# Optimization experiments

Measured on AMD Instinct MI355X. Metric: run time of the kernel, lower is better.

## Reference

```python
import jax, jax.numpy as jnp
import numpy as np

RANK = 8
LN_EPS = 1e-5


def setup_inputs() -> dict:
    key = jax.random.key(0)
    ks = jax.random.split(key, 8)
    B, T, D = 16, 1024, 1024
    A = 1024          # ada_dim
    I = 1024          # inter_dim
    OUT = D * RANK * 4  # 32768
    s = 0.02
    return {
        "x": jax.random.normal(ks[0], (B, T, D), jnp.float32),
        "ada_emb": jax.random.normal(ks[1], (B, A), jnp.float32),
        "base_up": jax.random.normal(ks[2], (D, D), jnp.float32) * s,
        "base_down": jax.random.normal(ks[3], (D, D), jnp.float32) * s,
        "ln_gamma": jnp.ones((A,), jnp.float32),
        "ln_beta": jnp.zeros((A,), jnp.float32),
        "W1": jax.random.normal(ks[4], (A, I), jnp.float32) / np.sqrt(A),
        "bias1": jnp.zeros((I,), jnp.float32),
        "W2": jax.random.normal(ks[5], (I, OUT), jnp.float32) / np.sqrt(I),
        "bias2": jnp.zeros((OUT,), jnp.float32),
    }


def reference(x, ada_emb, base_up, base_down, ln_gamma, ln_beta, W1, bias1, W2, bias2):
    B, T, D = x.shape
    R = RANK
    # norm_cond: LayerNorm over ada_dim (biased variance, eps=1e-5)
    mu = jnp.mean(ada_emb, axis=-1, keepdims=True)
    var = jnp.mean(jnp.square(ada_emb - mu), axis=-1, keepdims=True)
    c = (ada_emb - mu) / jnp.sqrt(var + LN_EPS) * ln_gamma + ln_beta
    # gen_weight: Linear -> GELU -> Linear
    h = jax.nn.gelu(c @ W1 + bias1, approximate=False)
    w = h @ W2 + bias2                         # (B, 4*D*R)
    a1, b1, a2, b2 = [t.reshape(B, D, R) for t in jnp.split(w, 4, axis=-1)]
    # down matvec: x @ (base_down + a2 @ b2^T), factored to avoid (B,D,D)
    u = jnp.einsum('btd,bdr->btr', x, a2)      # (B,T,R)
    mid = jnp.einsum('btd,dl->btl', x, base_down) + jnp.einsum('btr,blr->btl', u, b2)
    mid = jax.nn.gelu(mid, approximate=False)  # act_fn between layers
    # up matvec: (base_up + a1 @ b1^T) @ mid, factored
    v = jnp.einsum('blr,btl->btr', b1, mid)    # (B,T,R)
    out = jnp.einsum('btl,kl->btk', mid, base_up) + jnp.einsum('bkr,btr->btk', a1, v)
    return x + out  # residual
```

## Files before the change

### kernel.cpp

```cpp
#include <hip/hip_runtime.h>
#include <math.h>

#define DD 1024
#define NB 16
#define WSPLIT 8
#define HSPLIT 32

typedef unsigned short u16;
typedef __attribute__((ext_vector_type(8))) short short8;
typedef __attribute__((ext_vector_type(4))) float f32x4;

__device__ __forceinline__ float gelu_f(float x) {
  return 0.5f * x * (1.0f + erff(x * 0.70710678118654752440f));
}
__device__ __forceinline__ u16 f2bf(float f) {
  union { float f; unsigned u; } v; v.f = f;
  return (u16)((v.u + 0x7FFFu + ((v.u >> 16) & 1u)) >> 16);
}
__device__ __forceinline__ float bf2f(u16 b) {
  union { unsigned u; float f; } v; v.u = ((unsigned)b) << 16;
  return v.f;
}
__device__ __forceinline__ void gload_lds16(const u16* g, u16* l) {
  __builtin_amdgcn_global_load_lds(
      (const __attribute__((address_space(1))) void*)g,
      (__attribute__((address_space(3))) void*)l, 16, 0, 0);
}
__device__ __forceinline__ void gload_lds16f(const float* g, float* l) {
  __builtin_amdgcn_global_load_lds(
      (const __attribute__((address_space(1))) void*)g,
      (__attribute__((address_space(3))) void*)l, 16, 0, 0);
}

#define VMCNT8   asm volatile("s_waitcnt vmcnt(8)" ::: "memory")
#define VMCNT4   asm volatile("s_waitcnt vmcnt(4)" ::: "memory")
#define VMCNT0   asm volatile("s_waitcnt vmcnt(0)" ::: "memory")
#define BARRIER  asm volatile("s_barrier" ::: "memory")

__launch_bounds__(256)
__global__ void prep_kernel(const float* __restrict__ x, u16* __restrict__ xb,
                            const float* __restrict__ ada, const float* __restrict__ gamma,
                            const float* __restrict__ beta, float* __restrict__ c,
                            const float* __restrict__ bdn, u16* __restrict__ bdTb,
                            const float* __restrict__ bu, u16* __restrict__ bub) {
  __shared__ float smem[1056];
  int bid = blockIdx.x;
  int t = threadIdx.x;
  if (bid < 8192) {
    size_t i = (size_t)bid * 256 + t;
    const float4* xf = (const float4*)x;
    float4 v0 = xf[i * 2], v1 = xf[i * 2 + 1];
    short8 o;
    o[0] = (short)f2bf(v0.x); o[1] = (short)f2bf(v0.y);
    o[2] = (short)f2bf(v0.z); o[3] = (short)f2bf(v0.w);
    o[4] = (short)f2bf(v1.x); o[5] = (short)f2bf(v1.y);
    o[6] = (short)f2bf(v1.z); o[7] = (short)f2bf(v1.w);
    *(short8*)(xb + i * 8) = o;
  } else if (bid < 8208) {
    int b = bid - 8192;
    const float* row = ada + b * DD;
    float s = 0.f, s2 = 0.f;
    for (int i = t; i < DD; i += 256) { float v = row[i]; s += v; s2 += v * v; }
    for (int off = 32; off; off >>= 1) { s += __shfl_down(s, off); s2 += __shfl_down(s2, off); }
    float* rs = smem; float* rs2 = smem + 4;
    int wave = t >> 6, lane = t & 63;
    if (lane == 0) { rs[wave] = s; rs2[wave] = s2; }
    __syncthreads();
    if (t == 0) {
      float a = 0.f, a2 = 0.f;
      for (int w = 0; w < 4; w++) { a += rs[w]; a2 += rs2[w]; }
      rs[0] = a * (1.0f / DD); rs2[0] = a2 * (1.0f / DD);
    }
    __syncthreads();
    float mu = rs[0];
    float var = rs2[0] - mu * mu;
    float inv = rsqrtf(var + 1e-5f);
    for (int i = t; i < DD; i += 256)
      c[b * DD + i] = (row[i] - mu) * inv * gamma[i] + beta[i];
  } else if (bid < 9232) {
    int t2 = bid - 8208;
    int bx = (t2 & 31) * 32, by = (t2 >> 5) * 32;
    float (*tile)[33] = (float(*)[33])smem;
    int tx = t & 31, ty = t >> 5;
    for (int r = ty; r < 32; r += 8) tile[r][tx] = bdn[(size_t)(by + r) * DD + bx + tx];
    __syncthreads();
    for (int r = ty; r < 32; r += 8)
      bdTb[(size_t)(bx + r) * DD + by + tx] = f2bf(tile[tx][r]);
  } else {
    size_t i = (size_t)(bid - 9232) * 256 + t;
    const float4* bf = (const float4*)bu;
    float4 v0 = bf[i * 2], v1 = bf[i * 2 + 1];
    short8 o;
    o[0] = (short)f2bf(v0.x); o[1] = (short)f2bf(v0.y);
    o[2] = (short)f2bf(v0.z); o[3] = (short)f2bf(v0.w);
    o[4] = (short)f2bf(v1.x); o[5] = (short)f2bf(v1.y);
    o[6] = (short)f2bf(v1.z); o[7] = (short)f2bf(v1.w);
    *(short8*)(bub + i * 8) = o;
  }
}

__launch_bounds__(256)
__global__ void h_part_kernel(const float* __restrict__ c, const float* __restrict__ W1,
                              float* __restrict__ hpart) {
  int s = blockIdx.y;
  int j = blockIdx.x * 256 + threadIdx.x;
  int k0 = s * 32;
  __shared__ float cs[NB][32];
  for (int i = threadIdx.x; i < NB * 32; i += 256)
    cs[i >> 5][i & 31] = c[(size_t)(i >> 5) * DD + k0 + (i & 31)];
  __syncthreads();
  float acc[NB];
  #pragma unroll
  for (int b = 0; b < NB; b++) acc[b] = 0.f;
  #pragma unroll
  for (int al = 0; al < 32; al++) {
    float wv = W1[(size_t)(k0 + al) * DD + j];
    #pragma unroll
    for (int b = 0; b < NB; b++) acc[b] += cs[b][al] * wv;
  }
  #pragma unroll
  for (int b = 0; b < NB; b++)
    hpart[((size_t)s * NB + b) * DD + j] = acc[b];
}

__launch_bounds__(256)
__global__ void h_reduce_kernel(const float* __restrict__ hpart, const float* __restrict__ bias1,
                                float* __restrict__ h) {
  int idx = blockIdx.x * 256 + threadIdx.x;
  int j = idx & (DD - 1);
  float acc = bias1[j];
  #pragma unroll
  for (int s = 0; s < HSPLIT; s++) acc += hpart[(size_t)s * NB * DD + idx];
  h[idx] = gelu_f(acc);
}

#define WSTAGE(ST, BUF) do { int kr_ = k0 + (ST) * 4;                                  \
    _Pragma("unroll")                                                                  \
    for (int c_ = 0; c_ < 4; c_++)                                                     \
      gload_lds16f(W2 + (size_t)(kr_ + c_) * 32768 + j0 + t * 4,                       \
                   &wlds[BUF][c_][t * 4]);                                             \
  } while (0)

__launch_bounds__(256)
__global__ void w_part_kernel(const float* __restrict__ h, const float* __restrict__ W2,
                              float* __restrict__ part) {
  int s = blockIdx.y;
  int j0 = blockIdx.x * 1024;
  int k0 = s * 128;
  int t = threadIdx.x;
  __shared__ __align__(16) float wlds[2][4][1024];
  __shared__ __align__(16) float hlT[128][17];

  #pragma unroll
  for (int v = 0; v < 8; v++) {
    int i = t + v * 256;
    hlT[i & 127][i >> 7] = h[(size_t)(i >> 7) * DD + k0 + (i & 127)];
  }

  WSTAGE(0, 0);
  WSTAGE(1, 1);

  f32x4 acc[NB];
  #pragma unroll
  for (int b = 0; b < NB; b++) acc[b] = f32x4{0.f, 0.f, 0.f, 0.f};

  #pragma unroll 1
  for (int st = 0; st < 32; st++) {
    if (st < 31) { VMCNT4; } else { VMCNT0; }
    BARRIER;
    int buf = st & 1;
    #pragma unroll
    for (int r = 0; r < 4; r++) {
      f32x4 wv = *(const f32x4*)&wlds[buf][r][t * 4];
      int kk = st * 4 + r;
      f32x4 h0 = *(const f32x4*)&hlT[kk][0];
      f32x4 h1 = *(const f32x4*)&hlT[kk][4];
      f32x4 h2 = *(const f32x4*)&hlT[kk][8];
      f32x4 h3 = *(const f32x4*)&hlT[kk][12];
      #pragma unroll
      for (int q = 0; q < 4; q++) {
        acc[q]      += h0[q] * wv;
        acc[q + 4]  += h1[q] * wv;
        acc[q + 8]  += h2[q] * wv;
        acc[q + 12] += h3[q] * wv;
      }
    }
    BARRIER;
    if (st + 2 < 32) WSTAGE(st + 2, buf);
  }

  int j4 = blockIdx.x * 256 + t;
  f32x4* pv = (f32x4*)part;
  #pragma unroll
  for (int b = 0; b < NB; b++)
    pv[((size_t)s * NB + b) * 8192 + j4] = acc[b];
}

__launch_bounds__(256)
__global__ void pack_lora_kernel(const u16* __restrict__ src, const float* __restrict__ part,
                                 const float* __restrict__ bias2, int aoff, int boff,
                                 u16* __restrict__ aext, u16* __restrict__ bext) {
  int b = blockIdx.y;
  int t = threadIdx.x;
  int off = (blockIdx.x < 16) ? aoff : boff;
  __shared__ __align__(16) float fac[8192];
  for (int i = t; i < 8192; i += 256) {
    float acc = bias2[off + i];
    #pragma unroll
    for (int s = 0; s < WSPLIT; s++) acc += part[((size_t)s * NB + b) * 32768 + off + i];
    fac[i] = acc;
  }
  __syncthreads();
  short8 z = {};
  if (blockIdx.x < 16) {
    int row = blockIdx.x * 64 + (t >> 2);
    int q = t & 3;
    const u16* xr = src + ((size_t)b << 20) + (size_t)row * DD + q * 256;
    float acc[8] = {};
    #pragma unroll 2
    for (int kk = 0; kk < 32; kk++) {
      short8 xv = *(const short8*)(xr + kk * 8);
      #pragma unroll
      for (int e = 0; e < 8; e++) {
        float xf = bf2f((u16)xv[e]);
        int d = q * 256 + kk * 8 + e;
        f32x4 f0 = *(const f32x4*)&fac[d * 8];
        f32x4 f1 = *(const f32x4*)&fac[d * 8 + 4];
        acc[0] += xf * f0[0]; acc[1] += xf * f0[1];
        acc[2] += xf * f0[2]; acc[3] += xf * f0[3];
        acc[4] += xf * f1[0]; acc[5] += xf * f1[1];
        acc[6] += xf * f1[2]; acc[7] += xf * f1[3];
      }
    }
    #pragma unroll
    for (int r = 0; r < 8; r++) {
      acc[r] += __shfl_xor(acc[r], 1);
      acc[r] += __shfl_xor(acc[r], 2);
    }
    short8 ov = z;
    if (q == 0) {
      #pragma unroll
      for (int r = 0; r < 8; r++) ov[r] = (short)f2bf(acc[r]);
    }
    u16* orow = aext + ((size_t)b * 1024 + row) * 64 + q * 16;
    *(short8*)orow = ov;
    *(short8*)(orow + 8) = z;
  } else {
    for (int l = t; l < 1024; l += 256) {
      short8 ov;
      #pragma unroll
      for (int r = 0; r < 8; r++) ov[r] = (short)f2bf(fac[l * 8 + r]);
      u16* orow = bext + ((size_t)b * 1024 + l) * 64;
      *(short8*)orow = ov;
      #pragma unroll
      for (int k = 1; k < 8; k++) *(short8*)(orow + k * 8) = z;
    }
  }
}

#define STAGE_A(KT, BUF) do { int kt_ = (KT);                                          \
    if (kt_ < 16) { int ks_ = kt_ * 64;                                                \
      _Pragma("unroll")                                                                \
      for (int c_ = 0; c_ < 4; c_++)                                                   \
        gload_lds16(Ab + (size_t)srow[c_] * DD + ks_ + se[c_], As[BUF] + ldsel[c_]);   \
    } else {                                                                           \
      _Pragma("unroll")                                                                \
      for (int c_ = 0; c_ < 4; c_++)                                                   \
        gload_lds16(Ae + (size_t)srow[c_] * 64 + se[c_], As[BUF] + ldsel[c_]);         \
    } } while (0)
#define STAGE_B(KT, BUF) do { int kt_ = (KT);                                          \
    if (kt_ < 16) { int ks_ = kt_ * 64;                                                \
      _Pragma("unroll")                                                                \
      for (int c_ = 0; c_ < 4; c_++)                                                   \
        gload_lds16(Bb + (size_t)srow[c_] * DD + ks_ + se[c_], Bs[BUF] + ldsel[c_]);   \
    } else {                                                                           \
      _Pragma("unroll")                                                                \
      for (int c_ = 0; c_ < 4; c_++)                                                   \
        gload_lds16(Be + (size_t)srow[c_] * 64 + se[c_], Bs[BUF] + ldsel[c_]);         \
    } } while (0)

template<int PHASE>
__launch_bounds__(256, 2)
__global__ void gemm128_kernel(const u16* __restrict__ A, const u16* __restrict__ BT,
                               const u16* __restrict__ Aext, const u16* __restrict__ Bext,
                               const u16* __restrict__ resid, void* __restrict__ Cout) {
  constexpr int BK = 64;
  constexpr int NT = 17;
  __shared__ __align__(16) u16 As[2][128 * BK];
  __shared__ __align__(16) u16 Bs[2][128 * BK];

  int orig = blockIdx.x;
  int xcd = orig & 7, w = orig >> 3;
  int hb = (w >> 5) * 8 + xcd;
  int tile = w & 31;
  int b = hb >> 1;
  int tm = (hb & 1) * 4 + (tile >> 3);
  int tn = tile & 7;

  const u16* Ab = A + ((size_t)b << 20) + (size_t)(tm * 128) * DD;
  const u16* Bb = BT + (size_t)(tn * 128) * DD;
  const u16* Ae = Aext + ((size_t)b * 1024 + tm * 128) * 64;
  const u16* Be = Bext + ((size_t)b * 1024 + tn * 128) * 64;

  int t = threadIdx.x, lane = t & 63, g = lane >> 4, l15 = lane & 15;
  int wave = t >> 6;
  int wm = wave >> 1, wn = wave & 1;

  int srow[4], se[4], ldsel[4];
  #pragma unroll
  for (int c = 0; c < 4; c++) {
    int chunk = c * 256 + t;
    srow[c] = chunk >> 3;
    se[c] = ((chunk & 7) ^ (srow[c] & 7)) << 3;
    ldsel[c] = chunk * 8;
  }

  f32x4 acc[4][4] = {};

  STAGE_A(0, 0); STAGE_B(0, 0);
  STAGE_A(1, 1); STAGE_B(1, 1);
  VMCNT8;
  BARRIER;

  int cur = 0;
  #pragma unroll 1
  for (int kt = 0; kt < NT; kt++) {
    const u16* Ap = As[cur];
    const u16* Bp = Bs[cur];

    #pragma unroll
    for (int kk = 0; kk < 2; kk++) {
      short8 af[4], bf[4];
      #pragma unroll
      for (int i = 0; i < 4; i++) {
        int r = wm * 64 + i * 16 + l15;
        int e = (kk * 32 + g * 8) ^ ((r & 7) << 3);
        af[i] = *(const short8*)(Ap + r * BK + e);
      }
      #pragma unroll
      for (int j = 0; j < 4; j++) {
        int r = wn * 64 + j * 16 + l15;
        int e = (kk * 32 + g * 8) ^ ((r & 7) << 3);
        bf[j] = *(const short8*)(Bp + r * BK + e);
      }
      __builtin_amdgcn_s_setprio(1);
      #pragma unroll
      for (int i = 0; i < 4; i++)
        #pragma unroll
        for (int j = 0; j < 4; j++)
          acc[i][j] = __builtin_amdgcn_mfma_f32_16x16x32_bf16(af[i], bf[j], acc[i][j], 0, 0, 0);
      __builtin_amdgcn_s_setprio(0);
    }

    BARRIER;
    if (kt + 2 < NT) {
      STAGE_B(kt + 2, cur);
      STAGE_A(kt + 2, cur);
      VMCNT8;
    } else {
      VMCNT0;
    }
    BARRIER;

    cur ^= 1;
  }

  int r0 = tm * 128 + wm * 64, c0 = tn * 128 + wn * 64;
  if (PHASE == 1) {
    u16* mid = (u16*)Cout + ((size_t)b << 20);
    #pragma unroll
    for (int i = 0; i < 4; i++)
      #pragma unroll
      for (int j = 0; j < 4; j++)
        #pragma unroll
        for (int r = 0; r < 4; r++) {
          int row = r0 + i * 16 + g * 4 + r;
          int col = c0 + j * 16 + l15;
          mid[(size_t)row * DD + col] = f2bf(gelu_f(acc[i][j][r]));
        }
  } else {
    float* out = (float*)Cout + ((size_t)b << 20);
    const u16* xb = resid + ((size_t)b << 20);
    #pragma unroll
    for (int i = 0; i < 4; i++)
      #pragma unroll
      for (int j = 0; j < 4; j++)
        #pragma unroll
        for (int r = 0; r < 4; r++) {
          int row = r0 + i * 16 + g * 4 + r;
          int col = c0 + j * 16 + l15;
          size_t idx = (size_t)row * DD + col;
          out[idx] = bf2f(xb[idx]) + acc[i][j][r];
        }
  }
}

extern "C" void kernel_launch(void* const* d_in, const int* in_sizes, int n_in,
                              void* d_out, int out_size, void* d_ws, size_t ws_size,
                              hipStream_t stream) {
  const float* x         = (const float*)d_in[0];
  const float* ada       = (const float*)d_in[1];
  const float* base_up   = (const float*)d_in[2];
  const float* base_down = (const float*)d_in[3];
  const float* gamma     = (const float*)d_in[4];
  const float* beta      = (const float*)d_in[5];
  const float* W1        = (const float*)d_in[6];
  const float* bias1     = (const float*)d_in[7];
  const float* W2        = (const float*)d_in[8];
  const float* bias2     = (const float*)d_in[9];
  float* out = (float*)d_out;
  char* ws = (char*)d_ws;

  float* c     = (float*)(ws);
  float* h     = (float*)(ws + 0x10000);
  u16*   bdTb  = (u16*)  (ws + 0x220000);
  u16*   bub   = (u16*)  (ws + 0x420000);
  float* hpart = (float*)(ws + 0x620000);
  u16*   xb    = (u16*)  (ws + 0x820000);
  u16*   uext  = (u16*)  (ws + 0x2820000);
  u16*   b2ext = (u16*)  (ws + 0x2A20000);
  u16*   vext  = (u16*)  (ws + 0x2C20000);
  u16*   a1ext = (u16*)  (ws + 0x2E20000);
  u16*   mid   = (u16*)  (ws + 0x3020000);
  float* part  = (float*)(ws + 0x5020000);

  prep_kernel<<<dim3(9744), dim3(256), 0, stream>>>(x, xb, ada, gamma, beta, c,
                                                    base_down, bdTb, base_up, bub);
  h_part_kernel<<<dim3(4, HSPLIT), dim3(256), 0, stream>>>(c, W1, hpart);
  h_reduce_kernel<<<dim3(64), dim3(256), 0, stream>>>(hpart, bias1, h);
  w_part_kernel<<<dim3(32, WSPLIT), dim3(256), 0, stream>>>(h, W2, part);
  pack_lora_kernel<<<dim3(17, 16), dim3(256), 0, stream>>>(xb, part, bias2, 16384, 24576,
                                                           uext, b2ext);
  gemm128_kernel<1><<<dim3(1024), dim3(256), 0, stream>>>(xb, bdTb, uext, b2ext,
                                                          (const u16*)nullptr, (void*)mid);
  pack_lora_kernel<<<dim3(17, 16), dim3(256), 0, stream>>>(mid, part, bias2, 8192, 0,
                                                           vext, a1ext);
  gemm128_kernel<2><<<dim3(1024), dim3(256), 0, stream>>>(mid, bub, vext, a1ext, xb, (void*)out);
}
```

Measured before the change: 251.0 us.

## Single-buffer GEMM LDS tiles to raise occupancy; vectorize partial-sum reduction

The GEMM kernel drops its double-buffered LDS prefetch pipeline in favour of a single buffer: each k-step loads its tile, waits for all loads and synchronises before computing. Halving LDS per block lets the launch bound rise from 2 to 4 blocks per CU, so the intent is to hide latency through occupancy rather than software prefetch. In exchange, each block now exposes its global-load latency on every iteration, and register pressure must fit the tighter bound. The pack_lora reduction over split partials is also vectorised to float4 loads and stores.

```diff
diff --git a/kernel.cpp b/kernel.cpp
--- a/kernel.cpp
+++ b/kernel.cpp
@@ -32,7 +32,6 @@
       (__attribute__((address_space(3))) void*)l, 16, 0, 0);
 }
 
-#define VMCNT8   asm volatile("s_waitcnt vmcnt(8)" ::: "memory")
 #define VMCNT4   asm volatile("s_waitcnt vmcnt(4)" ::: "memory")
 #define VMCNT0   asm volatile("s_waitcnt vmcnt(0)" ::: "memory")
 #define BARRIER  asm volatile("s_barrier" ::: "memory")
@@ -204,11 +203,16 @@
   int t = threadIdx.x;
   int off = (blockIdx.x < 16) ? aoff : boff;
   __shared__ __align__(16) float fac[8192];
-  for (int i = t; i < 8192; i += 256) {
-    float acc = bias2[off + i];
-    #pragma unroll
-    for (int s = 0; s < WSPLIT; s++) acc += part[((size_t)s * NB + b) * 32768 + off + i];
-    fac[i] = acc;
+  {
+    const f32x4* bz = (const f32x4*)(bias2 + off);
+    #pragma unroll
+    for (int i4 = t; i4 < 2048; i4 += 256) {
+      f32x4 acc = bz[i4];
+      #pragma unroll
+      for (int s = 0; s < WSPLIT; s++)
+        acc += *(const f32x4*)(part + ((size_t)s * NB + b) * 32768 + off + i4 * 4);
+      *(f32x4*)&fac[i4 * 4] = acc;
+    }
   }
   __syncthreads();
   short8 z = {};
@@ -258,36 +262,36 @@
   }
 }
 
-#define STAGE_A(KT, BUF) do { int kt_ = (KT);                                          \
+#define STAGE_A(KT) do { int kt_ = (KT);                                               \
     if (kt_ < 16) { int ks_ = kt_ * 64;                                                \
       _Pragma("unroll")                                                                \
       for (int c_ = 0; c_ < 4; c_++)                                                   \
-        gload_lds16(Ab + (size_t)srow[c_] * DD + ks_ + se[c_], As[BUF] + ldsel[c_]);   \
+        gload_lds16(Ab + (size_t)srow[c_] * DD + ks_ + se[c_], As + ldsel[c_]);        \
     } else {                                                                           \
       _Pragma("unroll")                                                                \
       for (int c_ = 0; c_ < 4; c_++)                                                   \
-        gload_lds16(Ae + (size_t)srow[c_] * 64 + se[c_], As[BUF] + ldsel[c_]);         \
+        gload_lds16(Ae + (size_t)srow[c_] * 64 + se[c_], As + ldsel[c_]);              \
     } } while (0)
-#define STAGE_B(KT, BUF) do { int kt_ = (KT);                                          \
+#define STAGE_B(KT) do { int kt_ = (KT);                                               \
     if (kt_ < 16) { int ks_ = kt_ * 64;                                                \
       _Pragma("unroll")                                                                \
       for (int c_ = 0; c_ < 4; c_++)                                                   \
-        gload_lds16(Bb + (size_t)srow[c_] * DD + ks_ + se[c_], Bs[BUF] + ldsel[c_]);   \
+        gload_lds16(Bb + (size_t)srow[c_] * DD + ks_ + se[c_], Bs + ldsel[c_]);        \
     } else {                                                                           \
       _Pragma("unroll")                                                                \
       for (int c_ = 0; c_ < 4; c_++)                                                   \
-        gload_lds16(Be + (size_t)srow[c_] * 64 + se[c_], Bs[BUF] + ldsel[c_]);         \
+        gload_lds16(Be + (size_t)srow[c_] * 64 + se[c_], Bs + ldsel[c_]);              \
     } } while (0)
 
 template<int PHASE>
-__launch_bounds__(256, 2)
+__launch_bounds__(256, 4)
 __global__ void gemm128_kernel(const u16* __restrict__ A, const u16* __restrict__ BT,
                                const u16* __restrict__ Aext, const u16* __restrict__ Bext,
                                const u16* __restrict__ resid, void* __restrict__ Cout) {
   constexpr int BK = 64;
   constexpr int NT = 17;
-  __shared__ __align__(16) u16 As[2][128 * BK];
-  __shared__ __align__(16) u16 Bs[2][128 * BK];
+  __shared__ __align__(16) u16 As[128 * BK];
+  __shared__ __align__(16) u16 Bs[128 * BK];
 
   int orig = blockIdx.x;
   int xcd = orig & 7, w = orig >> 3;
@@ -317,17 +321,11 @@
 
   f32x4 acc[4][4] = {};
 
-  STAGE_A(0, 0); STAGE_B(0, 0);
-  STAGE_A(1, 1); STAGE_B(1, 1);
-  VMCNT8;
-  BARRIER;
-
-  int cur = 0;
   #pragma unroll 1
   for (int kt = 0; kt < NT; kt++) {
-    const u16* Ap = As[cur];
-    const u16* Bp = Bs[cur];
-
+    STAGE_A(kt); STAGE_B(kt);
+    VMCNT0;
+    BARRIER;
     #pragma unroll
     for (int kk = 0; kk < 2; kk++) {
       short8 af[4], bf[4];
@@ -335,13 +333,13 @@
       for (int i = 0; i < 4; i++) {
         int r = wm * 64 + i * 16 + l15;
         int e = (kk * 32 + g * 8) ^ ((r & 7) << 3);
-        af[i] = *(const short8*)(Ap + r * BK + e);
+        af[i] = *(const short8*)(As + r * BK + e);
       }
       #pragma unroll
       for (int j = 0; j < 4; j++) {
         int r = wn * 64 + j * 16 + l15;
         int e = (kk * 32 + g * 8) ^ ((r & 7) << 3);
-        bf[j] = *(const short8*)(Bp + r * BK + e);
+        bf[j] = *(const short8*)(Bs + r * BK + e);
       }
       __builtin_amdgcn_s_setprio(1);
       #pragma unroll
@@ -351,18 +349,7 @@
           acc[i][j] = __builtin_amdgcn_mfma_f32_16x16x32_bf16(af[i], bf[j], acc[i][j], 0, 0, 0);
       __builtin_amdgcn_s_setprio(0);
     }
-
     BARRIER;
-    if (kt + 2 < NT) {
-      STAGE_B(kt + 2, cur);
-      STAGE_A(kt + 2, cur);
-      VMCNT8;
-    } else {
-      VMCNT0;
-    }
-    BARRIER;
-
-    cur ^= 1;
   }
 
   int r0 = tm * 128 + wm * 64, c0 = tn * 128 + wn * 64;
```

New measurement: 242.6 us. 1.03x faster.
